# Kernel tuning notes

Measured on AMD Instinct MI355X. Metric: run time of the kernel, lower is better.

The kernel has to match this reference:

```python
import jax, jax.numpy as jnp
import numpy as np

B = 2048      # number of graphs
N = 256       # nodes per graph
D = 128       # node_embed_dim
H = 4         # num heads (subsets)
SUB = 32      # nodes per subset
DH = 128      # head_embed_dim
EPS = 1e-5


def setup_inputs() -> dict:
    key = jax.random.key(0)
    ks = jax.random.split(key, 4)
    subsets = np.concatenate([np.arange(h * 64, h * 64 + SUB) for h in range(H)])
    return {
        "node_embeddings": jax.random.normal(ks[0], (B * N, D), jnp.float32),
        "proj1_w": jax.random.normal(ks[1], (H, 3 * D, 2 * DH), jnp.float32) / np.float32(np.sqrt(3 * D)),
        "proj1_b": jnp.zeros((H, 2 * DH), jnp.float32),
        "gamma1": jnp.ones((2 * DH,), jnp.float32),
        "beta1": jnp.zeros((2 * DH,), jnp.float32),
        "proj2_w": jax.random.normal(ks[2], (H, 2 * DH, DH), jnp.float32) / np.float32(np.sqrt(2 * DH)),
        "proj2_b": jnp.zeros((H, DH), jnp.float32),
        "gamma2": jnp.ones((DH,), jnp.float32),
        "beta2": jnp.zeros((DH,), jnp.float32),
        "all_subset_nodes": jnp.asarray(subsets, jnp.int32),          # [H*SUB]
        "head_batch": jnp.asarray(np.repeat(np.arange(H), SUB), jnp.int32),  # [H*SUB]
        "batch": jnp.asarray(np.arange(B * N) // N, jnp.int32),      # [B*N] sorted graph ids
    }


def _layernorm(x, g, b):
    m = jnp.mean(x, axis=-1, keepdims=True)
    v = jnp.mean((x - m) ** 2, axis=-1, keepdims=True)
    return (x - m) * jax.lax.rsqrt(v + EPS) * g + b


def reference(node_embeddings, proj1_w, proj1_b, gamma1, beta1,
              proj2_w, proj2_b, gamma2, beta2,
              all_subset_nodes, head_batch, batch):
    # per-graph node offsets (mirrors torch bincount/cumsum path)
    counts_per_graph = jnp.bincount(batch, length=B)
    offsets = jnp.concatenate([jnp.zeros((1,), jnp.int32),
                               jnp.cumsum(counts_per_graph)[:-1].astype(jnp.int32)])
    flat_idx = offsets[:, None] + all_subset_nodes[None, :]   # [B, S]
    gathered = node_embeddings[flat_idx]                      # [B, S, D]

    # segment reductions over heads (sum, count, max)
    seg_sum = jax.vmap(lambda e: jax.ops.segment_sum(e, head_batch, num_segments=H))(gathered)  # [B,H,D]
    seg_max = jax.vmap(lambda e: jax.ops.segment_max(e, head_batch, num_segments=H))(gathered)  # [B,H,D]
    cnt = jax.ops.segment_sum(jnp.ones(head_batch.shape, jnp.float32), head_batch, num_segments=H)
    mean = seg_sum / jnp.clip(cnt, 1.0, None)[None, :, None]

    combined = jnp.concatenate([mean, seg_max, seg_sum], axis=-1)  # [B, H, 3D]

    h1 = jnp.einsum('bhi,hij->bhj', combined, proj1_w) + proj1_b
    h1 = jax.nn.relu(_layernorm(h1, gamma1, beta1))                # dropout is identity at eval
    out = jnp.einsum('bhi,hij->bhj', h1, proj2_w) + proj2_b
    out = jax.nn.relu(_layernorm(out, gamma2, beta2))
    return out                                                     # [B, H, DH]
```

## Files before the change

### kernel.cpp

```cpp
#include <hip/hip_runtime.h>
#include <math.h>

namespace {

constexpr int Bg   = 2048;
constexpr int Nn   = 256;
constexpr int Dd   = 128;
constexpr int Hh   = 4;
constexpr int SUBn = 32;
constexpr int DHd  = 128;
constexpr int D3   = 384;
constexpr int DH2  = 256;
constexpr int Gg   = 16;
constexpr int XP   = 392;
constexpr int HP   = 264;
constexpr float EPSf = 1e-5f;

typedef __attribute__((ext_vector_type(8))) short bf16x8;
typedef __attribute__((ext_vector_type(4))) float f32x4;

__device__ __forceinline__ unsigned short bf_rne(float f) {
    union { float f; unsigned int u; } v; v.f = f;
    const unsigned int u = v.u + 0x7FFFu + ((v.u >> 16) & 1u);
    return (unsigned short)(u >> 16);
}

__global__ __launch_bounds__(256)
void prep_k(const float* __restrict__ w1, const float* __restrict__ w2,
            const int* __restrict__ batch,
            unsigned short* __restrict__ wt1, unsigned short* __restrict__ wt2,
            int* __restrict__ offs)
{
    const int bid = (int)blockIdx.x;
    const int t   = (int)threadIdx.x;

    if (bid >= 128) {
        const int i = (bid - 128) * 256 + t;
        const int v = batch[i];
        if (i == 0 || batch[i - 1] != v) offs[v] = i;
        return;
    }

    __shared__ float tile[64][65];
    const float* src; unsigned short* dst; int K, J, k0, j0;
    if (bid < 96) {
        const int hb = bid / 24, tl = bid % 24;
        k0 = (tl % 6) * 64; j0 = (tl / 6) * 64;
        K = D3; J = DH2;
        src = w1 + (size_t)hb * D3 * DH2;
        dst = wt1 + (size_t)hb * DH2 * D3;
    } else {
        const int b2 = bid - 96, hb = b2 / 8, tl = b2 % 8;
        k0 = (tl % 4) * 64; j0 = (tl / 4) * 64;
        K = DH2; J = DHd;
        src = w2 + (size_t)hb * DH2 * DHd;
        dst = wt2 + (size_t)hb * DHd * DH2;
    }

    #pragma unroll
    for (int it = 0; it < 16; ++it) {
        const int idx = it * 256 + t;
        tile[idx >> 6][idx & 63] =
            src[(size_t)(k0 + (idx >> 6)) * J + (j0 + (idx & 63))];
    }
    __syncthreads();
    #pragma unroll
    for (int it = 0; it < 16; ++it) {
        const int idx = it * 256 + t;
        const int jr = idx >> 6, kc = idx & 63;
        dst[(size_t)(j0 + jr) * K + (k0 + kc)] = bf_rne(tile[kc][jr]);
    }
}

__global__ __launch_bounds__(256, 4)
void gather_k(const float* __restrict__ emb,
              const int* __restrict__ subset,
              const int* __restrict__ offs,
              unsigned short* __restrict__ comb)
{
    __shared__ int sn[Hh * SUBn];
    const int t = (int)threadIdx.x;
    if (t < Hh * SUBn) sn[t] = subset[t];
    __syncthreads();

    const int b    = (int)blockIdx.x;
    const int h    = t >> 6;
    const int lane = t & 63;
    const int half = lane >> 5;
    const int c    = lane & 31;

    const float* base = emb + (size_t)offs[b] * Dd + c * 4;

    float sx = 0.f, sy = 0.f, sz = 0.f, sw = 0.f;
    float mxx = -INFINITY, mxy = -INFINITY, mxz = -INFINITY, mxw = -INFINITY;
    #pragma unroll
    for (int s2 = 0; s2 < 16; ++s2) {
        const int r = sn[h * SUBn + 2 * s2 + half];
        const float4 v = *reinterpret_cast<const float4*>(base + (size_t)r * Dd);
        sx += v.x; sy += v.y; sz += v.z; sw += v.w;
        mxx = fmaxf(mxx, v.x); mxy = fmaxf(mxy, v.y);
        mxz = fmaxf(mxz, v.z); mxw = fmaxf(mxw, v.w);
    }

    sx += __shfl_xor(sx, 32, 64);
    sy += __shfl_xor(sy, 32, 64);
    sz += __shfl_xor(sz, 32, 64);
    sw += __shfl_xor(sw, 32, 64);
    mxx = fmaxf(mxx, __shfl_xor(mxx, 32, 64));
    mxy = fmaxf(mxy, __shfl_xor(mxy, 32, 64));
    mxz = fmaxf(mxz, __shfl_xor(mxz, 32, 64));
    mxw = fmaxf(mxw, __shfl_xor(mxw, 32, 64));

    unsigned short* dst = comb + ((size_t)b * Hh + h) * D3 + c * 4;
    if (half == 0) {
        *reinterpret_cast<ushort4*>(dst) =
            make_ushort4(bf_rne(sx * 0.03125f), bf_rne(sy * 0.03125f),
                         bf_rne(sz * 0.03125f), bf_rne(sw * 0.03125f));
        *reinterpret_cast<ushort4*>(dst + Dd) =
            make_ushort4(bf_rne(mxx), bf_rne(mxy), bf_rne(mxz), bf_rne(mxw));
    } else {
        *reinterpret_cast<ushort4*>(dst + 2 * Dd) =
            make_ushort4(bf_rne(sx), bf_rne(sy), bf_rne(sz), bf_rne(sw));
    }
}

__global__ __launch_bounds__(256, 2)
void mlp_k(const unsigned short* __restrict__ comb,
           const unsigned short* __restrict__ wt1,
           const unsigned short* __restrict__ wt2,
           const float* __restrict__ b1, const float* __restrict__ g1,
           const float* __restrict__ be1,
           const float* __restrict__ b2, const float* __restrict__ g2,
           const float* __restrict__ be2,
           float* __restrict__ out)
{
    __shared__ __align__(16) unsigned short X[Gg * XP];
    __shared__ __align__(16) unsigned short H1s[Gg * HP];
    __shared__ float red[2][4][Gg];

    const int t   = (int)threadIdx.x;
    const int bid = (int)blockIdx.x;
    const int xcd = bid & 7, slot = bid >> 3;
    const int head = xcd >> 1;
    const int gblk = ((xcd & 1) << 6) + slot;
    const int gbase = gblk * Gg;

    {
        const int g = t >> 4, i = t & 15;
        const uint4* s4 = reinterpret_cast<const uint4*>(
            comb + ((size_t)(gbase + g) * Hh + head) * D3 + i * 24);
        uint4* d4 = reinterpret_cast<uint4*>(X + g * XP + i * 24);
        d4[0] = s4[0]; d4[1] = s4[1]; d4[2] = s4[2];
    }
    __syncthreads();

    const int lane = t & 63, wv = t >> 6;
    const int lrow = lane & 15, q = lane >> 4;

    bf16x8 a1[12];
    #pragma unroll
    for (int k0 = 0; k0 < 12; ++k0)
        a1[k0] = *reinterpret_cast<const bf16x8*>(X + lrow * XP + k0 * 32 + q * 8);

    f32x4 acc[4];
    #pragma unroll
    for (int jt = 0; jt < 4; ++jt) {
        const int j = wv * 64 + jt * 16 + lrow;
        const float bj = b1[head * DH2 + j];
        f32x4 c = {bj, bj, bj, bj};
        const unsigned short* wp = wt1 + ((size_t)head * DH2 + j) * D3 + q * 8;
        #pragma unroll
        for (int k0 = 0; k0 < 12; ++k0)
            c = __builtin_amdgcn_mfma_f32_16x16x32_bf16(
                    a1[k0], *reinterpret_cast<const bf16x8*>(wp + k0 * 32), c, 0, 0, 0);
        acc[jt] = c;
    }

    {
        float s1[4], s2[4];
        #pragma unroll
        for (int r = 0; r < 4; ++r) {
            float a = acc[0][r] + acc[1][r] + acc[2][r] + acc[3][r];
            float b = acc[0][r] * acc[0][r] + acc[1][r] * acc[1][r]
                    + acc[2][r] * acc[2][r] + acc[3][r] * acc[3][r];
            #pragma unroll
            for (int m = 1; m < 16; m <<= 1) {
                a += __shfl_xor(a, m, 64);
                b += __shfl_xor(b, m, 64);
            }
            s1[r] = a; s2[r] = b;
        }
        if (lrow == 0) {
            #pragma unroll
            for (int r = 0; r < 4; ++r) {
                red[0][wv][q * 4 + r] = s1[r];
                red[1][wv][q * 4 + r] = s2[r];
            }
        }
        __syncthreads();

        float t1[4] = {0.f, 0.f, 0.f, 0.f}, t2[4] = {0.f, 0.f, 0.f, 0.f};
        #pragma unroll
        for (int w = 0; w < 4; ++w) {
            const float4 r1 = *reinterpret_cast<const float4*>(&red[0][w][q * 4]);
            const float4 r2 = *reinterpret_cast<const float4*>(&red[1][w][q * 4]);
            t1[0] += r1.x; t1[1] += r1.y; t1[2] += r1.z; t1[3] += r1.w;
            t2[0] += r2.x; t2[1] += r2.y; t2[2] += r2.z; t2[3] += r2.w;
        }
        float mean[4], rstd[4];
        #pragma unroll
        for (int r = 0; r < 4; ++r) {
            mean[r] = t1[r] * (1.f / 256.f);
            const float var = t2[r] * (1.f / 256.f) - mean[r] * mean[r];
            rstd[r] = rsqrtf(var + EPSf);
        }
        #pragma unroll
        for (int jt = 0; jt < 4; ++jt) {
            const int j = wv * 64 + jt * 16 + lrow;
            const float gj = g1[j], bj = be1[j];
            #pragma unroll
            for (int r = 0; r < 4; ++r) {
                const float h = fmaxf(0.f, (acc[jt][r] - mean[r]) * rstd[r] * gj + bj);
                H1s[(q * 4 + r) * HP + j] = bf_rne(h);
            }
        }
    }
    __syncthreads();

    bf16x8 a2[8];
    #pragma unroll
    for (int k0 = 0; k0 < 8; ++k0)
        a2[k0] = *reinterpret_cast<const bf16x8*>(H1s + lrow * HP + k0 * 32 + q * 8);

    f32x4 acc2[2];
    #pragma unroll
    for (int jt = 0; jt < 2; ++jt) {
        const int j = wv * 32 + jt * 16 + lrow;
        const float bj = b2[head * DHd + j];
        f32x4 c = {bj, bj, bj, bj};
        const unsigned short* wp = wt2 + ((size_t)head * DHd + j) * DH2 + q * 8;
        #pragma unroll
        for (int k0 = 0; k0 < 8; ++k0)
            c = __builtin_amdgcn_mfma_f32_16x16x32_bf16(
                    a2[k0], *reinterpret_cast<const bf16x8*>(wp + k0 * 32), c, 0, 0, 0);
        acc2[jt] = c;
    }

    {
        float s1[4], s2[4];
        #pragma unroll
        for (int r = 0; r < 4; ++r) {
            float a = acc2[0][r] + acc2[1][r];
            float b = acc2[0][r] * acc2[0][r] + acc2[1][r] * acc2[1][r];
            #pragma unroll
            for (int m = 1; m < 16; m <<= 1) {
                a += __shfl_xor(a, m, 64);
                b += __shfl_xor(b, m, 64);
            }
            s1[r] = a; s2[r] = b;
        }
        __syncthreads();
        if (lrow == 0) {
            #pragma unroll
            for (int r = 0; r < 4; ++r) {
                red[0][wv][q * 4 + r] = s1[r];
                red[1][wv][q * 4 + r] = s2[r];
            }
        }
        __syncthreads();

        float t1[4] = {0.f, 0.f, 0.f, 0.f}, t2[4] = {0.f, 0.f, 0.f, 0.f};
        #pragma unroll
        for (int w = 0; w < 4; ++w) {
            const float4 r1 = *reinterpret_cast<const float4*>(&red[0][w][q * 4]);
            const float4 r2 = *reinterpret_cast<const float4*>(&red[1][w][q * 4]);
            t1[0] += r1.x; t1[1] += r1.y; t1[2] += r1.z; t1[3] += r1.w;
            t2[0] += r2.x; t2[1] += r2.y; t2[2] += r2.z; t2[3] += r2.w;
        }
        #pragma unroll
        for (int r = 0; r < 4; ++r) {
            const float mean = t1[r] * (1.f / 128.f);
            const float var  = t2[r] * (1.f / 128.f) - mean * mean;
            const float rstd = rsqrtf(var + EPSf);
            #pragma unroll
            for (int jt = 0; jt < 2; ++jt) {
                const int j = wv * 32 + jt * 16 + lrow;
                const float o = fmaxf(0.f,
                    (acc2[jt][r] - mean) * rstd * g2[j] + be2[j]);
                out[(size_t)(gbase + q * 4 + r) * (Hh * DHd) + head * DHd + j] = o;
            }
        }
    }
}

}

extern "C" void kernel_launch(void* const* d_in, const int* in_sizes, int n_in,
                              void* d_out, int out_size, void* d_ws, size_t ws_size,
                              hipStream_t stream) {
    const float* emb  = (const float*)d_in[0];
    const float* w1   = (const float*)d_in[1];
    const float* b1   = (const float*)d_in[2];
    const float* g1   = (const float*)d_in[3];
    const float* be1  = (const float*)d_in[4];
    const float* w2   = (const float*)d_in[5];
    const float* b2   = (const float*)d_in[6];
    const float* g2   = (const float*)d_in[7];
    const float* be2  = (const float*)d_in[8];
    const int* subset = (const int*)d_in[9];
    const int* batch  = (const int*)d_in[11];
    float* out = (float*)d_out;

    int* offs = (int*)d_ws;
    unsigned short* wt1 = (unsigned short*)((char*)d_ws + 16384);
    unsigned short* wt2 = wt1 + (size_t)Hh * DH2 * D3;
    unsigned short* comb = wt2 + (size_t)Hh * DHd * DH2;

    prep_k  <<<dim3(128 + Bg * Nn / 256), dim3(256), 0, stream>>>(w1, w2, batch,
                                                                  wt1, wt2, offs);
    gather_k<<<dim3(Bg), dim3(256), 0, stream>>>(emb, subset, offs, comb);
    mlp_k   <<<dim3(Hh * (Bg / Gg)), dim3(256), 0, stream>>>(comb, wt1, wt2,
                                                             b1, g1, be1,
                                                             b2, g2, be2, out);
}
```

Baseline: 49.72 us.

## Fuse subset gather and segment reductions into the MLP kernel

Removes the separate gather kernel and its bf16 intermediate buffer in global memory. Each MLP block now gathers the 32 subset rows for its 16 graphs and one head, computes mean, max and sum in registers, and writes them straight into the shared X tile. This saves one kernel launch and a write/read round trip of the combined features. In exchange the fused kernel's launch bounds change from 2 to 4 blocks per SM, which may cap registers for the MLP part. The gather is also now spread over only 512 blocks instead of 2048, each thread making 32 serial iterations, so memory parallelism may drop.

```diff
diff --git a/kernel.cpp b/kernel.cpp
--- a/kernel.cpp
+++ b/kernel.cpp
@@ -73,70 +73,22 @@
 }
 
 __global__ __launch_bounds__(256, 4)
-void gather_k(const float* __restrict__ emb,
-              const int* __restrict__ subset,
-              const int* __restrict__ offs,
-              unsigned short* __restrict__ comb)
-{
-    __shared__ int sn[Hh * SUBn];
-    const int t = (int)threadIdx.x;
-    if (t < Hh * SUBn) sn[t] = subset[t];
-    __syncthreads();
-
-    const int b    = (int)blockIdx.x;
-    const int h    = t >> 6;
-    const int lane = t & 63;
-    const int half = lane >> 5;
-    const int c    = lane & 31;
-
-    const float* base = emb + (size_t)offs[b] * Dd + c * 4;
-
-    float sx = 0.f, sy = 0.f, sz = 0.f, sw = 0.f;
-    float mxx = -INFINITY, mxy = -INFINITY, mxz = -INFINITY, mxw = -INFINITY;
-    #pragma unroll
-    for (int s2 = 0; s2 < 16; ++s2) {
-        const int r = sn[h * SUBn + 2 * s2 + half];
-        const float4 v = *reinterpret_cast<const float4*>(base + (size_t)r * Dd);
-        sx += v.x; sy += v.y; sz += v.z; sw += v.w;
-        mxx = fmaxf(mxx, v.x); mxy = fmaxf(mxy, v.y);
-        mxz = fmaxf(mxz, v.z); mxw = fmaxf(mxw, v.w);
-    }
-
-    sx += __shfl_xor(sx, 32, 64);
-    sy += __shfl_xor(sy, 32, 64);
-    sz += __shfl_xor(sz, 32, 64);
-    sw += __shfl_xor(sw, 32, 64);
-    mxx = fmaxf(mxx, __shfl_xor(mxx, 32, 64));
-    mxy = fmaxf(mxy, __shfl_xor(mxy, 32, 64));
-    mxz = fmaxf(mxz, __shfl_xor(mxz, 32, 64));
-    mxw = fmaxf(mxw, __shfl_xor(mxw, 32, 64));
-
-    unsigned short* dst = comb + ((size_t)b * Hh + h) * D3 + c * 4;
-    if (half == 0) {
-        *reinterpret_cast<ushort4*>(dst) =
-            make_ushort4(bf_rne(sx * 0.03125f), bf_rne(sy * 0.03125f),
-                         bf_rne(sz * 0.03125f), bf_rne(sw * 0.03125f));
-        *reinterpret_cast<ushort4*>(dst + Dd) =
-            make_ushort4(bf_rne(mxx), bf_rne(mxy), bf_rne(mxz), bf_rne(mxw));
-    } else {
-        *reinterpret_cast<ushort4*>(dst + 2 * Dd) =
-            make_ushort4(bf_rne(sx), bf_rne(sy), bf_rne(sz), bf_rne(sw));
-    }
-}
-
-__global__ __launch_bounds__(256, 2)
-void mlp_k(const unsigned short* __restrict__ comb,
-           const unsigned short* __restrict__ wt1,
-           const unsigned short* __restrict__ wt2,
-           const float* __restrict__ b1, const float* __restrict__ g1,
-           const float* __restrict__ be1,
-           const float* __restrict__ b2, const float* __restrict__ g2,
-           const float* __restrict__ be2,
-           float* __restrict__ out)
+void fused_k(const float* __restrict__ emb,
+             const unsigned short* __restrict__ wt1,
+             const unsigned short* __restrict__ wt2,
+             const int* __restrict__ subset,
+             const int* __restrict__ offs,
+             const float* __restrict__ b1, const float* __restrict__ g1,
+             const float* __restrict__ be1,
+             const float* __restrict__ b2, const float* __restrict__ g2,
+             const float* __restrict__ be2,
+             float* __restrict__ out)
 {
     __shared__ __align__(16) unsigned short X[Gg * XP];
     __shared__ __align__(16) unsigned short H1s[Gg * HP];
     __shared__ float red[2][4][Gg];
+    __shared__ int sn[SUBn];
+    __shared__ int soff[Gg];
 
     const int t   = (int)threadIdx.x;
     const int bid = (int)blockIdx.x;
@@ -145,12 +97,49 @@
     const int gblk = ((xcd & 1) << 6) + slot;
     const int gbase = gblk * Gg;
 
+    if (t < SUBn) sn[t] = subset[head * SUBn + t];
+    if (t >= 64 && t < 64 + Gg) soff[t - 64] = offs[gbase + (t - 64)];
+    __syncthreads();
+
     {
-        const int g = t >> 4, i = t & 15;
-        const uint4* s4 = reinterpret_cast<const uint4*>(
-            comb + ((size_t)(gbase + g) * Hh + head) * D3 + i * 24);
-        uint4* d4 = reinterpret_cast<uint4*>(X + g * XP + i * 24);
-        d4[0] = s4[0]; d4[1] = s4[1]; d4[2] = s4[2];
+        const int g  = t >> 4;
+        const int cp = t & 15;
+        const float* base = emb + (size_t)soff[g] * Dd;
+
+        float sAx = 0.f, sAy = 0.f, sAz = 0.f, sAw = 0.f;
+        float sBx = 0.f, sBy = 0.f, sBz = 0.f, sBw = 0.f;
+        float mAx = -INFINITY, mAy = -INFINITY, mAz = -INFINITY, mAw = -INFINITY;
+        float mBx = -INFINITY, mBy = -INFINITY, mBz = -INFINITY, mBw = -INFINITY;
+
+        #pragma unroll 4
+        for (int s = 0; s < SUBn; ++s) {
+            const float* rp = base + (size_t)sn[s] * Dd;
+            const float4 va = *reinterpret_cast<const float4*>(rp + cp * 4);
+            const float4 vb = *reinterpret_cast<const float4*>(rp + cp * 4 + 64);
+            sAx += va.x; sAy += va.y; sAz += va.z; sAw += va.w;
+            sBx += vb.x; sBy += vb.y; sBz += vb.z; sBw += vb.w;
+            mAx = fmaxf(mAx, va.x); mAy = fmaxf(mAy, va.y);
+            mAz = fmaxf(mAz, va.z); mAw = fmaxf(mAw, va.w);
+            mBx = fmaxf(mBx, vb.x); mBy = fmaxf(mBy, vb.y);
+            mBz = fmaxf(mBz, vb.z); mBw = fmaxf(mBw, vb.w);
+        }
+
+        unsigned short* xr = X + g * XP;
+        const int dA = cp * 4, dB = cp * 4 + 64;
+        *reinterpret_cast<ushort4*>(xr + dA) =
+            make_ushort4(bf_rne(sAx * 0.03125f), bf_rne(sAy * 0.03125f),
+                         bf_rne(sAz * 0.03125f), bf_rne(sAw * 0.03125f));
+        *reinterpret_cast<ushort4*>(xr + dB) =
+            make_ushort4(bf_rne(sBx * 0.03125f), bf_rne(sBy * 0.03125f),
+                         bf_rne(sBz * 0.03125f), bf_rne(sBw * 0.03125f));
+        *reinterpret_cast<ushort4*>(xr + Dd + dA) =
+            make_ushort4(bf_rne(mAx), bf_rne(mAy), bf_rne(mAz), bf_rne(mAw));
+        *reinterpret_cast<ushort4*>(xr + Dd + dB) =
+            make_ushort4(bf_rne(mBx), bf_rne(mBy), bf_rne(mBz), bf_rne(mBw));
+        *reinterpret_cast<ushort4*>(xr + 2 * Dd + dA) =
+            make_ushort4(bf_rne(sAx), bf_rne(sAy), bf_rne(sAz), bf_rne(sAw));
+        *reinterpret_cast<ushort4*>(xr + 2 * Dd + dB) =
+            make_ushort4(bf_rne(sBx), bf_rne(sBy), bf_rne(sBz), bf_rne(sBw));
     }
     __syncthreads();
 
@@ -314,12 +303,11 @@
     int* offs = (int*)d_ws;
     unsigned short* wt1 = (unsigned short*)((char*)d_ws + 16384);
     unsigned short* wt2 = wt1 + (size_t)Hh * DH2 * D3;
-    unsigned short* comb = wt2 + (size_t)Hh * DHd * DH2;
-
-    prep_k  <<<dim3(128 + Bg * Nn / 256), dim3(256), 0, stream>>>(w1, w2, batch,
-                                                                  wt1, wt2, offs);
-    gather_k<<<dim3(Bg), dim3(256), 0, stream>>>(emb, subset, offs, comb);
-    mlp_k   <<<dim3(Hh * (Bg / Gg)), dim3(256), 0, stream>>>(comb, wt1, wt2,
-                                                             b1, g1, be1,
-                                                             b2, g2, be2, out);
-}
+
+    prep_k <<<dim3(128 + Bg * Nn / 256), dim3(256), 0, stream>>>(w1, w2, batch,
+                                                                 wt1, wt2, offs);
+    fused_k<<<dim3(Hh * (Bg / Gg)), dim3(256), 0, stream>>>(emb, wt1, wt2,
+                                                            subset, offs,
+                                                            b1, g1, be1,
+                                                            b2, g2, be2, out);
+}
```

Measured after the change: 46.05 us. 7.4% less time.
